# Kernel optimization log

Hardware: AMD Instinct MI355X
Metric: run time of the kernel (lower is better)

The kernel has to match this reference:

```python
import jax, jax.numpy as jnp
import numpy as np

N = 8000   # nodes
E = 32000  # edges
B = 64     # graphs in batch
V = 5000   # vocab
D = 200    # embed dim; 20 tokens/node * 200 = 4000 = conv1 in_dim
T = 20


def setup_inputs() -> dict:
    key = jax.random.key(0)
    ks = jax.random.split(key, 12)
    return {
        "x": jax.random.randint(ks[0], (N, T), 0, V),
        "edge_index": jax.random.randint(ks[1], (2, E), 0, N),
        "batch": jnp.sort(jax.random.randint(ks[2], (N,), 0, B)),
        "emb": jax.random.normal(ks[3], (V, D), jnp.float32) * 0.02,
        "W1": jax.random.normal(ks[4], (4000, 6000), jnp.float32) * 0.01,
        "b1": jnp.zeros((6000,), jnp.float32),
        "W2": jax.random.normal(ks[5], (6000, 6000), jnp.float32) * 0.01,
        "b2": jnp.zeros((6000,), jnp.float32),
        "Wl1": jax.random.normal(ks[6], (6000, 3000), jnp.float32) * 0.01,
        "bl1": jnp.zeros((3000,), jnp.float32),
        "Wl2": jax.random.normal(ks[7], (3000, 4), jnp.float32) * 0.01,
        "bl2": jnp.zeros((4,), jnp.float32),
    }


def gcn_conv(h, W, b, src, dst, n):
    """PyG GCNConv: x' = D^-1/2 (A+I) D^-1/2 (x W) + b; src/dst include self-loops."""
    h = h @ W  # [n, out]
    deg = jax.ops.segment_sum(jnp.ones(dst.shape[0], h.dtype), dst, num_segments=n)
    dinv = jnp.where(deg > 0, jax.lax.rsqrt(deg), 0.0)
    norm = dinv[src] * dinv[dst]  # [E+n]
    agg = jax.ops.segment_sum(h[src] * norm[:, None], dst, num_segments=n)
    return agg + b


def reference(x, edge_index, batch, emb, W1, b1, W2, b2, Wl1, bl1, Wl2, bl2):
    n = x.shape[0]
    h = emb[x].reshape(n, -1)  # [N, 4000]
    loops = jnp.arange(n)
    src = jnp.concatenate([edge_index[0], loops])
    dst = jnp.concatenate([edge_index[1], loops])
    h = jax.nn.leaky_relu(gcn_conv(h, W1, b1, src, dst, n))  # dropout: identity in eval
    h = jax.nn.leaky_relu(gcn_conv(h, W2, b2, src, dst, n))
    g = jax.ops.segment_max(h, batch, num_segments=B)  # global_max_pool -> [B, 6000]
    g = jax.nn.leaky_relu(g @ Wl1 + bl1)
    return jax.nn.leaky_relu(g @ Wl2 + bl2)  # [B, 4]
```

## Files before the change

kernel.cpp:

```cpp
#include <hip/hip_runtime.h>
#include <hip/hip_bf16.h>

#define Nn 8000
#define Ee 32000
#define Bb 64
#define Dembed 200
#define Ttok 20
#define Mp 8192
#define K1 4096
#define K1L 4032
#define K2 6144
#define K2L 6016
#define L1p 3072
#define LCHUNK 256
#define NCH 24

#define GBM 256
#define GBN 256
#define GBK 64
#define ABUF (GBM * GBK)
#define BUFE (2 * ABUF)

#define LRELU(v) ((v) > 0.f ? (v) : 0.01f * (v))

typedef __attribute__((ext_vector_type(4))) float f32x4;
typedef __attribute__((ext_vector_type(8))) short s16x8;
typedef __attribute__((ext_vector_type(4))) short s16x4;

#define GLL16(gp, lp) __builtin_amdgcn_global_load_lds( \
    (const __attribute__((address_space(1))) void*)(gp), \
    (__attribute__((address_space(3))) void*)(lp), 16, 0, 0)

__device__ __forceinline__ float b2f(short s) {
    union { unsigned u; float f; } c;
    c.u = ((unsigned)(unsigned short)s) << 16;
    return c.f;
}
__device__ __forceinline__ short f2b(float f) {
    __hip_bfloat16 h = __float2bfloat16(f);
    return __builtin_bit_cast(short, h);
}

__global__ void k_deg(const int* __restrict__ dst, int* __restrict__ indeg) {
    int e = blockIdx.x * 256 + threadIdx.x;
    if (e < Ee) atomicAdd(&indeg[dst[e]], 1);
}

__global__ __launch_bounds__(1024)
void k_scan(const int* __restrict__ indeg, int* __restrict__ rowptr,
            float* __restrict__ dinv, int n)
{
    __shared__ int sums[1024];
    const int t = threadIdx.x;
    const int base = t * 8;
    int loc[8];
    int s = 0;
#pragma unroll
    for (int j = 0; j < 8; ++j) {
        int v = (base + j < n) ? indeg[base + j] : 0;
        loc[j] = s; s += v;
    }
    sums[t] = s;
    __syncthreads();
    for (int off = 1; off < 1024; off <<= 1) {
        int v = sums[t];
        int add = (t >= off) ? sums[t - off] : 0;
        __syncthreads();
        sums[t] = v + add;
        __syncthreads();
    }
    const int prev = (t == 0) ? 0 : sums[t - 1];
#pragma unroll
    for (int j = 0; j < 8; ++j)
        if (base + j < n) {
            rowptr[base + j] = prev + loc[j];
            dinv[base + j] = rsqrtf((float)indeg[base + j] + 1.0f);
        }
    if (t == 1023) rowptr[n] = sums[1023];
}

__global__ void k_fill(const int* __restrict__ src, const int* __restrict__ dst,
                       const int* __restrict__ rowptr, int* __restrict__ fillc,
                       int* __restrict__ csr) {
    int e = blockIdx.x * 256 + threadIdx.x;
    if (e < Ee) {
        int d = dst[e];
        int pos = rowptr[d] + atomicAdd(&fillc[d], 1);
        csr[pos] = src[e];
    }
}

__global__ __launch_bounds__(256)
void k_gagg(const int* __restrict__ x, const float* __restrict__ emb,
            const float* __restrict__ dinv, const int* __restrict__ rowptr,
            const int* __restrict__ csr, short* __restrict__ Ah0)
{
    const int i = blockIdx.x;
    const int tid = threadIdx.x;
    __shared__ float s_w[64];
    __shared__ int s_tok[64 * Ttok];
    __shared__ int s_tok0[Ttok];

    int cg[2], tk0[2], off0[2], nsp[2];
    bool valid[2];
#pragma unroll
    for (int g = 0; g < 2; ++g) {
        cg[g] = tid * 8 + g * 2048;
        valid[g] = (cg[g] < Ttok * Dembed);
        tk0[g] = cg[g] / Dembed;
        off0[g] = cg[g] - tk0[g] * Dembed;
        int r = Dembed - off0[g];
        nsp[g] = r > 8 ? 8 : r;
    }

    const float di = dinv[i];
    const float wself = di * di;

    if (tid < Ttok) s_tok0[tid] = x[i * Ttok + tid];
    __syncthreads();

    float acc[2][8] = {};
#pragma unroll
    for (int g = 0; g < 2; ++g) {
        if (!valid[g]) continue;
        const float* r0 = emb + (long)s_tok0[tk0[g]] * Dembed + off0[g];
        for (int j = 0; j < nsp[g]; ++j) acc[g][j] = wself * r0[j];
        if (nsp[g] < 8) {
            const float* r1 = emb + (long)s_tok0[tk0[g] + 1] * Dembed + (off0[g] - Dembed);
            for (int j = nsp[g]; j < 8; ++j) acc[g][j] = wself * r1[j];
        }
    }

    const int e0 = rowptr[i], e1 = rowptr[i + 1];
    for (int eb = e0; eb < e1; eb += 64) {
        const int cnt = min(64, e1 - eb);
        __syncthreads();
        if (tid < cnt) {
            int s = csr[eb + tid];
            s_w[tid] = dinv[s] * di;
        }
        __syncthreads();
        for (int f = tid; f < cnt * Ttok; f += 256) {
            int e = f / Ttok;
            int tk = f - e * Ttok;
            s_tok[f] = x[(long)csr[eb + e] * Ttok + tk];
        }
        __syncthreads();
        for (int e = 0; e < cnt; ++e) {
            const float w = s_w[e];
            const int* te = s_tok + e * Ttok;
#pragma unroll
            for (int g = 0; g < 2; ++g) {
                if (!valid[g]) continue;
                const float* r0 = emb + (long)te[tk0[g]] * Dembed + off0[g];
                for (int j = 0; j < nsp[g]; ++j) acc[g][j] += w * r0[j];
                if (nsp[g] < 8) {
                    const float* r1 = emb + (long)te[tk0[g] + 1] * Dembed + (off0[g] - Dembed);
                    for (int j = nsp[g]; j < 8; ++j) acc[g][j] += w * r1[j];
                }
            }
        }
    }

#pragma unroll
    for (int g = 0; g < 2; ++g) {
        s16x8 o;
#pragma unroll
        for (int j = 0; j < 8; ++j) o[j] = f2b(acc[g][j]);
        *(s16x8*)(Ah0 + (long)i * K1 + cg[g]) = o;
    }
}

template<int NG>
__global__ __launch_bounds__(256)
void k_agg(const short* __restrict__ Hin, short* __restrict__ Hout,
           const float* __restrict__ dinv, const int* __restrict__ rowptr,
           const int* __restrict__ csr, int Wp)
{
    const int i = blockIdx.x;
    const int tid = threadIdx.x;
    __shared__ int   s_idx[64];
    __shared__ float s_w[64];
    const float di = dinv[i];
    const float wself = di * di;
    const long rowi = (long)i * Wp;
    float acc[NG * 8];
#pragma unroll
    for (int gI = 0; gI < NG; ++gI) {
        s16x8 v = *(const s16x8*)(Hin + rowi + gI * 2048 + tid * 8);
#pragma unroll
        for (int j = 0; j < 8; ++j) acc[gI * 8 + j] = wself * b2f(v[j]);
    }
    const int e0 = rowptr[i], e1 = rowptr[i + 1];
    for (int eb = e0; eb < e1; eb += 64) {
        const int cnt = min(64, e1 - eb);
        __syncthreads();
        if (tid < cnt) {
            int s = csr[eb + tid];
            s_idx[tid] = s;
            s_w[tid] = dinv[s] * di;
        }
        __syncthreads();
        for (int e = 0; e < cnt; ++e) {
            const long rows = (long)s_idx[e] * Wp;
            const float w = s_w[e];
#pragma unroll
            for (int gI = 0; gI < NG; ++gI) {
                s16x8 v = *(const s16x8*)(Hin + rows + gI * 2048 + tid * 8);
#pragma unroll
                for (int j = 0; j < 8; ++j) acc[gI * 8 + j] += w * b2f(v[j]);
            }
        }
    }
#pragma unroll
    for (int gI = 0; gI < NG; ++gI) {
        s16x8 o;
#pragma unroll
        for (int j = 0; j < 8; ++j) o[j] = f2b(acc[gI * 8 + j]);
        *(s16x8*)(Hout + rowi + gI * 2048 + tid * 8) = o;
    }
}

__global__ __launch_bounds__(256)
void k_transpose(const float* __restrict__ In, short* __restrict__ Out,
                 int K, int N, int Kp, int Np)
{
    __shared__ float tile[32][33];
    const int k0 = blockIdx.x * 32;
    const int n0 = blockIdx.y * 32;
    const int tid = threadIdx.x;
    const int ln = tid & 31, lk = tid >> 5;
#pragma unroll
    for (int kk = lk; kk < 32; kk += 8) {
        int k = k0 + kk, n = n0 + ln;
        tile[kk][ln] = (k < K && n < N) ? In[(long)k * N + n] : 0.f;
    }
    __syncthreads();
    const int kq = tid & 7, nn = tid >> 3;
    s16x4 o;
#pragma unroll
    for (int j = 0; j < 4; ++j) o[j] = f2b(tile[kq * 4 + j][nn]);
    *(s16x4*)(&Out[(long)(n0 + nn) * Kp + k0 + kq * 4]) = o;
}

__global__ __launch_bounds__(512, 2)
void k_gemm8w(const short* __restrict__ A, const short* __restrict__ Bt,
              short* __restrict__ C, const float* __restrict__ bias,
              int K, int Kloop, int Np, int Nreal, int nbx)
{
    __shared__ short lds[2 * BUFE];

    const int tid  = threadIdx.x;
    const int lane = tid & 63;
    const int wid  = tid >> 6;
    const int wm   = wid >> 2;
    const int wn   = wid & 3;

    const int cpx = (int)gridDim.x >> 3;
    const int bid = (int)blockIdx.x;
    const int swz = (bid & 7) * cpx + (bid >> 3);
    const int bx = swz % nbx;
    const int by = swz / nbx;

    const int rq = tid >> 3;
    const int kq = ((tid & 7) << 3) ^ ((rq & 7) << 3);
    const short* Abase = A  + ((long)by * GBM + rq) * K + kq;
    const short* Bbase = Bt + ((long)bx * GBN + rq) * K + kq;

#define ST2(bb, t2, base, ldoff, c0_, c1_) do { \
    const short* g0_ = (base) + (long)((c0_) * 64) * K + (long)(t2) * GBK; \
    const short* g1_ = (base) + (long)((c1_) * 64) * K + (long)(t2) * GBK; \
    GLL16(g0_, lds + (bb) * BUFE + (ldoff) + (c0_) * 4096 + tid * 8); \
    GLL16(g1_, lds + (bb) * BUFE + (ldoff) + (c1_) * 4096 + tid * 8); \
  } while (0)

    const int fr  = lane & 15;
    const int kb8 = (lane >> 4) << 3;
    const int xm  = (fr & 7) << 3;
    const int ck0 = kb8 ^ xm;
    const int ck1 = (32 + kb8) ^ xm;
    const int aoff = (wm * 128 + fr) * 64;
    const int boff = ABUF + (wn * 64 + fr) * 64;

    f32x4 acc[8][4] = {};
    s16x8 av_a[4], av_b[4], bv1[4], bv3[4];

    const int NT = Kloop >> 6;

    ST2(0, 0, Bbase, ABUF, 0, 1);
    ST2(0, 0, Bbase, ABUF, 2, 3);
    ST2(0, 0, Abase, 0,    0, 2);
    ST2(0, 0, Abase, 0,    1, 3);
    asm volatile("s_waitcnt vmcnt(0)" ::: "memory");
    __builtin_amdgcn_s_barrier();

    int buf = 0;
    for (int t = 0; t < NT; ++t) {
        const short* lb = lds + buf * BUFE;
        const int nb = buf ^ 1;
        const bool pf = (t + 1 < NT);

#pragma unroll
        for (int n = 0; n < 4; ++n) bv1[n] = *(const s16x8*)(lb + boff + n * 1024 + ck0);
#pragma unroll
        for (int m = 0; m < 4; ++m) av_a[m] = *(const s16x8*)(lb + aoff + m * 1024 + ck0);
        if (pf) ST2(nb, t + 1, Bbase, ABUF, 0, 1);
#pragma unroll
        for (int m = 0; m < 4; ++m) av_b[m] = *(const s16x8*)(lb + aoff + (4 + m) * 1024 + ck0);
        __builtin_amdgcn_s_setprio(1);
#pragma unroll
        for (int m = 0; m < 4; ++m)
#pragma unroll
            for (int n = 0; n < 4; ++n)
                acc[m][n] = __builtin_amdgcn_mfma_f32_16x16x32_bf16(av_a[m], bv1[n], acc[m][n], 0, 0, 0);
        __builtin_amdgcn_s_setprio(0);
        if (pf) ST2(nb, t + 1, Bbase, ABUF, 2, 3);
#pragma unroll
        for (int n = 0; n < 4; ++n) bv3[n] = *(const s16x8*)(lb + boff + n * 1024 + ck1);
#pragma unroll
        for (int m = 0; m < 4; ++m) av_a[m] = *(const s16x8*)(lb + aoff + (4 + m) * 1024 + ck1);
        __builtin_amdgcn_s_setprio(1);
#pragma unroll
        for (int m = 0; m < 4; ++m)
#pragma unroll
            for (int n = 0; n < 4; ++n)
                acc[4 + m][n] = __builtin_amdgcn_mfma_f32_16x16x32_bf16(av_b[m], bv1[n], acc[4 + m][n], 0, 0, 0);
        __builtin_amdgcn_s_setprio(0);
        if (pf) ST2(nb, t + 1, Abase, 0, 0, 2);
#pragma unroll
        for (int m = 0; m < 4; ++m) av_b[m] = *(const s16x8*)(lb + aoff + m * 1024 + ck1);
        __builtin_amdgcn_s_setprio(1);
#pragma unroll
        for (int m = 0; m < 4; ++m)
#pragma unroll
            for (int n = 0; n < 4; ++n)
                acc[4 + m][n] = __builtin_amdgcn_mfma_f32_16x16x32_bf16(av_a[m], bv3[n], acc[4 + m][n], 0, 0, 0);
        __builtin_amdgcn_s_setprio(0);
        if (pf) ST2(nb, t + 1, Abase, 0, 1, 3);
        __builtin_amdgcn_s_setprio(1);
#pragma unroll
        for (int m = 0; m < 4; ++m)
#pragma unroll
            for (int n = 0; n < 4; ++n)
                acc[m][n] = __builtin_amdgcn_mfma_f32_16x16x32_bf16(av_b[m], bv3[n], acc[m][n], 0, 0, 0);
        __builtin_amdgcn_s_setprio(0);

        asm volatile("s_waitcnt vmcnt(0)" ::: "memory");
        __builtin_amdgcn_s_barrier();
        buf = nb;
    }

    const int rr = (lane >> 4) << 2;
    long colv[4];
    float bb[4];
#pragma unroll
    for (int n = 0; n < 4; ++n) {
        colv[n] = (long)bx * GBN + wn * 64 + n * 16 + fr;
        bb[n] = (colv[n] < Nreal) ? bias[colv[n]] : 0.f;
    }
#pragma unroll
    for (int m = 0; m < 8; ++m) {
#pragma unroll
        for (int j = 0; j < 4; ++j) {
            const long rowoff = ((long)by * GBM + wm * 128 + m * 16 + rr + j) * Np;
#pragma unroll
            for (int n = 0; n < 4; ++n) {
                float v = acc[m][n][j] + bb[n];
                v = LRELU(v);
                C[rowoff + colv[n]] = f2b(v);
            }
        }
    }
#undef ST2
}

__global__ void k_bptr(const int* __restrict__ batch, int* __restrict__ bptr) {
    int i = blockIdx.x * 256 + threadIdx.x;
    if (i >= Nn) return;
    int b = batch[i];
    int pb = (i == 0) ? -1 : batch[i - 1];
    for (int bb = pb + 1; bb <= b; ++bb) bptr[bb] = i;
    if (i == Nn - 1)
        for (int bb = b + 1; bb <= Bb; ++bb) bptr[bb] = Nn;
}

__global__ __launch_bounds__(256)
void k_pool(const short* __restrict__ h2, const int* __restrict__ bptr,
            float* __restrict__ g, int Wp) {
    const int c8 = blockIdx.x * 256 + threadIdx.x;
    const int b = blockIdx.y;
    const short* base = h2 + (long)c8 * 8;
    float mx[8];
#pragma unroll
    for (int j = 0; j < 8; ++j) mx[j] = -INFINITY;
    const int i0 = bptr[b], i1 = bptr[b + 1];
    for (int i = i0; i < i1; ++i) {
        s16x8 v = *(const s16x8*)(base + (long)i * Wp);
#pragma unroll
        for (int j = 0; j < 8; ++j) mx[j] = fmaxf(mx[j], b2f(v[j]));
    }
#pragma unroll
    for (int j = 0; j < 8; ++j) g[(long)b * Wp + c8 * 8 + j] = mx[j];
}

__global__ __launch_bounds__(256)
void k_lin1_part(const float* __restrict__ g, const float* __restrict__ Wl1,
                 float* __restrict__ part) {
    __shared__ float gs[64][65];
    __shared__ float Ws[64][64];
    const int tid = threadIdx.x;
    const int jc = blockIdx.x * 64;
    const int k0 = blockIdx.y * LCHUNK;
    const int k1 = min(6000, k0 + LCHUNK);
    const int r = tid & 63;
    const int jb = (tid >> 6) * 16;
    float acc[16] = {};
    for (int kc = k0; kc < k1; kc += 64) {
#pragma unroll
        for (int p = 0; p < 16; ++p) {
            int el = p * 256 + tid;
            int rr = el >> 6, kk = el & 63;
            gs[rr][kk] = (kc + kk < k1) ? g[rr * K2 + kc + kk] : 0.f;
            Ws[rr][kk] = (kc + rr < k1 && jc + kk < 3000)
                         ? Wl1[(long)(kc + rr) * 3000 + jc + kk] : 0.f;
        }
        __syncthreads();
#pragma unroll
        for (int k = 0; k < 64; ++k) {
            float a = gs[r][k];
#pragma unroll
            for (int jj = 0; jj < 16; ++jj)
                acc[jj] += a * Ws[k][jb + jj];
        }
        __syncthreads();
    }
    float* prow = part + ((long)blockIdx.y * 64 + r) * L1p + jc + jb;
#pragma unroll
    for (int jj = 0; jj < 16; ++jj) prow[jj] = acc[jj];
}

__global__ __launch_bounds__(256)
void k_lin1_red(const float* __restrict__ part, const float* __restrict__ bl1,
                float* __restrict__ g1) {
    int idx = blockIdx.x * 256 + threadIdx.x;
    if (idx >= 64 * 3000) return;
    int r = idx / 3000;
    int c = idx - r * 3000;
    float s = bl1[c];
#pragma unroll
    for (int p = 0; p < NCH; ++p)
        s += part[((long)p * 64 + r) * L1p + c];
    g1[r * L1p + c] = LRELU(s);
}

__global__ __launch_bounds__(256)
void k_lin2(const float* __restrict__ g1, const float* __restrict__ Wl2,
            const float* __restrict__ bl2, float* __restrict__ out) {
    const int r = blockIdx.x;
    const int tid = threadIdx.x;
    float a0 = 0, a1 = 0, a2 = 0, a3 = 0;
    for (int k = tid; k < 3000; k += 256) {
        float gv = g1[r * L1p + k];
        const float* w = Wl2 + (long)k * 4;
        a0 += gv * w[0]; a1 += gv * w[1]; a2 += gv * w[2]; a3 += gv * w[3];
    }
    __shared__ float red[256][4];
    red[tid][0] = a0; red[tid][1] = a1; red[tid][2] = a2; red[tid][3] = a3;
    __syncthreads();
    for (int s = 128; s > 0; s >>= 1) {
        if (tid < s) {
            red[tid][0] += red[tid + s][0]; red[tid][1] += red[tid + s][1];
            red[tid][2] += red[tid + s][2]; red[tid][3] += red[tid + s][3];
        }
        __syncthreads();
    }
    if (tid < 4) {
        float v = red[0][tid] + bl2[tid];
        out[r * 4 + tid] = LRELU(v);
    }
}

extern "C" void kernel_launch(void* const* d_in, const int* in_sizes, int n_in,
                              void* d_out, int out_size, void* d_ws, size_t ws_size,
                              hipStream_t stream)
{
    const int*   x     = (const int*)d_in[0];
    const int*   ei    = (const int*)d_in[1];
    const int*   batch = (const int*)d_in[2];
    const float* emb   = (const float*)d_in[3];
    const float* W1    = (const float*)d_in[4];
    const float* b1    = (const float*)d_in[5];
    const float* W2    = (const float*)d_in[6];
    const float* b2    = (const float*)d_in[7];
    const float* Wl1   = (const float*)d_in[8];
    const float* bl1   = (const float*)d_in[9];
    const float* Wl2   = (const float*)d_in[10];
    const float* bl2   = (const float*)d_in[11];
    float* out = (float*)d_out;

    const int* esrc = ei;
    const int* edst = ei + Ee;

    const size_t MiB = 1ull << 20;
    char* W = (char*)d_ws;
    short* Ah0b = (short*)(W + 64 * MiB);
    short* W2t  = (short*)(W + 96 * MiB);
    short* W1t  = (short*)(W + 128 * MiB);
    short* h1b  = (short*)(W + 176 * MiB);
    short* Ah1b = (short*)(W + 0);
    short* h2b  = h1b;
    float* part = (float*)(W + 0);
    char* S = W + 272 * MiB;
    int*   indeg  = (int*)(S);
    int*   fillc  = (int*)(S + 32 * 1024);
    int*   rowptr = (int*)(S + 64 * 1024);
    float* dinv   = (float*)(S + 96 * 1024);
    int*   csr    = (int*)(S + 128 * 1024);
    int*   bptr   = (int*)(S + 256 * 1024);
    float* g      = (float*)(S + 320 * 1024);
    float* g1     = (float*)(S + 320 * 1024 + 2 * MiB);

    hipMemsetAsync(indeg, 0, 64 * 1024, stream);

    k_deg<<<(Ee + 255) / 256, 256, 0, stream>>>(edst, indeg);
    k_scan<<<1, 1024, 0, stream>>>(indeg, rowptr, dinv, Nn);
    k_fill<<<(Ee + 255) / 256, 256, 0, stream>>>(esrc, edst, rowptr, fillc, csr);

    const int nbx = K2 / GBN;
    const int nwg = nbx * (Mp / GBM);

    k_gagg<<<Nn, 256, 0, stream>>>(x, emb, dinv, rowptr, csr, Ah0b);
    k_transpose<<<dim3(K1 / 32, K2 / 32), 256, 0, stream>>>(W1, W1t, 4000, 6000, K1, K2);
    k_gemm8w<<<nwg, 512, 0, stream>>>(Ah0b, W1t, h1b, b1, K1, K1L, K2, 6000, nbx);

    k_transpose<<<dim3(K2 / 32, K2 / 32), 256, 0, stream>>>(W2, W2t, 6000, 6000, K2, K2);
    k_agg<3><<<Nn, 256, 0, stream>>>(h1b, Ah1b, dinv, rowptr, csr, K2);
    k_gemm8w<<<nwg, 512, 0, stream>>>(Ah1b, W2t, h2b, b2, K2, K2L, K2, 6000, nbx);

    k_bptr<<<(Nn + 255) / 256, 256, 0, stream>>>(batch, bptr);
    k_pool<<<dim3(K2 / 2048, Bb), 256, 0, stream>>>(h2b, bptr, g, K2);
    k_lin1_part<<<dim3(L1p / 64, NCH), 256, 0, stream>>>(g, Wl1, part);
    k_lin1_red<<<(64 * 3000 + 255) / 256, 256, 0, stream>>>(part, bl1, g1);
    k_lin2<<<Bb, 256, 0, stream>>>(g1, Wl2, bl2, out);
}
```

Before: 1.347 ms.

## Vectorize embedding gather, pair edges in aggregation, reorder GEMM prefetch issue

The embedding-gather kernel now reads each 8-float span as two 16-byte vector loads. This relies on the 8-column groups never crossing a 200-wide token boundary, which holds because 200 is a multiple of 8. The aggregation kernel processes two neighbor rows per iteration so more global loads are in flight before accumulation. In the GEMM main loop, the global-to-LDS prefetch stores are issued before each MFMA block rather than after it, to overlap them with compute. The trade-off is higher register pressure.

```diff
diff --git a/kernel.cpp b/kernel.cpp
--- a/kernel.cpp
+++ b/kernel.cpp
@@ -101,7 +101,7 @@
     __shared__ int s_tok[64 * Ttok];
     __shared__ int s_tok0[Ttok];
 
-    int cg[2], tk0[2], off0[2], nsp[2];
+    int cg[2], tk0[2], off0[2];
     bool valid[2];
 #pragma unroll
     for (int g = 0; g < 2; ++g) {
@@ -109,8 +109,6 @@
         valid[g] = (cg[g] < Ttok * Dembed);
         tk0[g] = cg[g] / Dembed;
         off0[g] = cg[g] - tk0[g] * Dembed;
-        int r = Dembed - off0[g];
-        nsp[g] = r > 8 ? 8 : r;
     }
 
     const float di = dinv[i];
@@ -123,12 +121,10 @@
 #pragma unroll
     for (int g = 0; g < 2; ++g) {
         if (!valid[g]) continue;
-        const float* r0 = emb + (long)s_tok0[tk0[g]] * Dembed + off0[g];
-        for (int j = 0; j < nsp[g]; ++j) acc[g][j] = wself * r0[j];
-        if (nsp[g] < 8) {
-            const float* r1 = emb + (long)s_tok0[tk0[g] + 1] * Dembed + (off0[g] - Dembed);
-            for (int j = nsp[g]; j < 8; ++j) acc[g][j] = wself * r1[j];
-        }
+        const f32x4* r = (const f32x4*)(emb + (long)s_tok0[tk0[g]] * Dembed + off0[g]);
+        f32x4 v0 = r[0], v1 = r[1];
+#pragma unroll
+        for (int j = 0; j < 4; ++j) { acc[g][j] = wself * v0[j]; acc[g][4 + j] = wself * v1[j]; }
     }
 
     const int e0 = rowptr[i], e1 = rowptr[i + 1];
@@ -152,12 +148,10 @@
 #pragma unroll
             for (int g = 0; g < 2; ++g) {
                 if (!valid[g]) continue;
-                const float* r0 = emb + (long)te[tk0[g]] * Dembed + off0[g];
-                for (int j = 0; j < nsp[g]; ++j) acc[g][j] += w * r0[j];
-                if (nsp[g] < 8) {
-                    const float* r1 = emb + (long)te[tk0[g] + 1] * Dembed + (off0[g] - Dembed);
-                    for (int j = nsp[g]; j < 8; ++j) acc[g][j] += w * r1[j];
-                }
+                const f32x4* r = (const f32x4*)(emb + (long)te[tk0[g]] * Dembed + off0[g]);
+                f32x4 v0 = r[0], v1 = r[1];
+#pragma unroll
+                for (int j = 0; j < 4; ++j) { acc[g][j] += w * v0[j]; acc[g][4 + j] += w * v1[j]; }
             }
         }
     }
@@ -201,14 +195,31 @@
             s_w[tid] = dinv[s] * di;
         }
         __syncthreads();
-        for (int e = 0; e < cnt; ++e) {
-            const long rows = (long)s_idx[e] * Wp;
-            const float w = s_w[e];
+        int e = 0;
+        for (; e + 1 < cnt; e += 2) {
+            const long ra = (long)s_idx[e] * Wp;
+            const long rb = (long)s_idx[e + 1] * Wp;
+            const float wa = s_w[e], wb = s_w[e + 1];
+            s16x8 va[NG], vb[NG];
 #pragma unroll
             for (int gI = 0; gI < NG; ++gI) {
-                s16x8 v = *(const s16x8*)(Hin + rows + gI * 2048 + tid * 8);
-#pragma unroll
-                for (int j = 0; j < 8; ++j) acc[gI * 8 + j] += w * b2f(v[j]);
+                va[gI] = *(const s16x8*)(Hin + ra + gI * 2048 + tid * 8);
+                vb[gI] = *(const s16x8*)(Hin + rb + gI * 2048 + tid * 8);
+            }
+#pragma unroll
+            for (int gI = 0; gI < NG; ++gI)
+#pragma unroll
+                for (int j = 0; j < 8; ++j)
+                    acc[gI * 8 + j] += wa * b2f(va[gI][j]) + wb * b2f(vb[gI][j]);
+        }
+        if (e < cnt) {
+            const long ra = (long)s_idx[e] * Wp;
+            const float wa = s_w[e];
+#pragma unroll
+            for (int gI = 0; gI < NG; ++gI) {
+                s16x8 v = *(const s16x8*)(Hin + ra + gI * 2048 + tid * 8);
+#pragma unroll
+                for (int j = 0; j < 8; ++j) acc[gI * 8 + j] += wa * b2f(v[j]);
             }
         }
     }
@@ -307,6 +318,7 @@
         if (pf) ST2(nb, t + 1, Bbase, ABUF, 0, 1);
 #pragma unroll
         for (int m = 0; m < 4; ++m) av_b[m] = *(const s16x8*)(lb + aoff + (4 + m) * 1024 + ck0);
+        if (pf) ST2(nb, t + 1, Bbase, ABUF, 2, 3);
         __builtin_amdgcn_s_setprio(1);
 #pragma unroll
         for (int m = 0; m < 4; ++m)
@@ -314,11 +326,11 @@
             for (int n = 0; n < 4; ++n)
                 acc[m][n] = __builtin_amdgcn_mfma_f32_16x16x32_bf16(av_a[m], bv1[n], acc[m][n], 0, 0, 0);
         __builtin_amdgcn_s_setprio(0);
-        if (pf) ST2(nb, t + 1, Bbase, ABUF, 2, 3);
 #pragma unroll
         for (int n = 0; n < 4; ++n) bv3[n] = *(const s16x8*)(lb + boff + n * 1024 + ck1);
 #pragma unroll
         for (int m = 0; m < 4; ++m) av_a[m] = *(const s16x8*)(lb + aoff + (4 + m) * 1024 + ck1);
+        if (pf) ST2(nb, t + 1, Abase, 0, 0, 2);
         __builtin_amdgcn_s_setprio(1);
 #pragma unroll
         for (int m = 0; m < 4; ++m)
@@ -326,9 +338,9 @@
             for (int n = 0; n < 4; ++n)
                 acc[4 + m][n] = __builtin_amdgcn_mfma_f32_16x16x32_bf16(av_b[m], bv1[n], acc[4 + m][n], 0, 0, 0);
         __builtin_amdgcn_s_setprio(0);
-        if (pf) ST2(nb, t + 1, Abase, 0, 0, 2);
 #pragma unroll
         for (int m = 0; m < 4; ++m) av_b[m] = *(const s16x8*)(lb + aoff + m * 1024 + ck1);
+        if (pf) ST2(nb, t + 1, Abase, 0, 1, 3);
         __builtin_amdgcn_s_setprio(1);
 #pragma unroll
         for (int m = 0; m < 4; ++m)
@@ -336,7 +348,6 @@
             for (int n = 0; n < 4; ++n)
                 acc[4 + m][n] = __builtin_amdgcn_mfma_f32_16x16x32_bf16(av_a[m], bv3[n], acc[4 + m][n], 0, 0, 0);
         __builtin_amdgcn_s_setprio(0);
-        if (pf) ST2(nb, t + 1, Abase, 0, 1, 3);
         __builtin_amdgcn_s_setprio(1);
 #pragma unroll
         for (int m = 0; m < 4; ++m)
```

New measurement: 1.268 ms. 1.06x faster.
